# Kernel tuning notes

Measured on AMD Instinct MI355X. Metric: run time of the kernel, lower is better.

## Reference

```python
import jax, jax.numpy as jnp
import numpy as np


def setup_inputs() -> dict:
    key = jax.random.key(0)
    ks = jax.random.split(key, 6)
    B, L, N, C, D = 8, 512, 2048, 1024, 128
    return {
        "teacher_logits": jax.random.normal(ks[0], (B, L, N), dtype=jnp.float32),
        "teacher_features": jax.random.normal(ks[1], (B, N, C), dtype=jnp.float32),
        "Wq": jax.random.normal(ks[2], (D, C), dtype=jnp.float32) * (1.0 / np.sqrt(C)),
        "bq": jnp.zeros((D,), dtype=jnp.float32),
        "Wk": jax.random.normal(ks[3], (D, C), dtype=jnp.float32) * (1.0 / np.sqrt(C)),
        "bk": jnp.zeros((D,), dtype=jnp.float32),
    }


def reference(teacher_logits, teacher_features, Wq, bq, Wk, bk):
    # Linear projections (torch nn.Linear: x @ W^T + b)
    query = jnp.einsum("bnc,dc->bnd", teacher_features, Wq) + bq  # [B,N,D]
    key = jnp.einsum("bnc,dc->bnd", teacher_features, Wk) + bk    # [B,N,D]
    energy = jnp.einsum("bnd,bmd->bnm", query, key)               # [B,N,N]
    attention = jax.nn.softmax(energy, axis=-1)                   # softmax over last dim
    # x_m = teacher_logits @ attention^T : [B,L,N] x [B,N,N]^T -> [B,L,N]
    x_m = jnp.einsum("bln,bmn->blm", teacher_logits, attention)
    return x_m
```

## Files before the change

### kernel.cpp

```cpp
#include <hip/hip_runtime.h>
#include <hip/hip_bf16.h>

#define B_ 8
#define L_ 512
#define N_ 2048
#define C_ 1024
#define D_ 128

typedef __attribute__((ext_vector_type(8))) short    short8;
typedef __attribute__((ext_vector_type(8))) _Float16 half8;
typedef __attribute__((ext_vector_type(4))) float    floatx4;

static __device__ __forceinline__ float s2f(short s) {
    return __uint_as_float(((unsigned)(unsigned short)s) << 16);
}
static __device__ __forceinline__ short f2bf(float f) {
    union { __hip_bfloat16 h; short s; } u;
    u.h = __float2bfloat16(f);
    return u.s;
}

struct F8 { float v[8]; };

static __device__ __forceinline__ F8 load8(const void* raw, long off, int is_bf16) {
    F8 r;
    if (is_bf16) {
        short8 x = *reinterpret_cast<const short8*>((const short*)raw + off);
        #pragma unroll
        for (int i = 0; i < 8; ++i) r.v[i] = s2f(x[i]);
    } else {
        const float* p = (const float*)raw + off;
        float4 a = *reinterpret_cast<const float4*>(p);
        float4 b = *reinterpret_cast<const float4*>(p + 4);
        r.v[0]=a.x; r.v[1]=a.y; r.v[2]=a.z; r.v[3]=a.w;
        r.v[4]=b.x; r.v[5]=b.y; r.v[6]=b.z; r.v[7]=b.w;
    }
    return r;
}

static __device__ __forceinline__ float bias_at(const void* raw, int d, int is_bf16) {
    return is_bf16 ? s2f(((const short*)raw)[d]) : ((const float*)raw)[d];
}

static __device__ __forceinline__ void load_lds16(const void* g, void* l) {
    __builtin_amdgcn_global_load_lds(
        (const __attribute__((address_space(1))) void*)g,
        (__attribute__((address_space(3))) void*)l, 16, 0, 0);
}

__global__ void detect_kernel(const unsigned* __restrict__ words, int* __restrict__ flag) {
    int cnt = 0;
    for (int i = threadIdx.x; i < 256; i += 64) {
        float lowv = __uint_as_float(words[i] << 16);
        float a = fabsf(lowv);
        if (a >= 1e-5f && a <= 100.0f) cnt++;
    }
    #pragma unroll
    for (int off = 32; off; off >>= 1) cnt += __shfl_down(cnt, off);
    if (threadIdx.x == 0) flag[0] = (cnt > 128) ? 1 : 0;
}

__global__ __launch_bounds__(1024) void zero_kernel(float* __restrict__ Z, int n) {
    int i = blockIdx.x * 1024 + threadIdx.x;
    if (i < n) Z[i] = 0.0f;
}

__global__ __launch_bounds__(256) void cvt_kernel(const void* __restrict__ in_raw,
                                                  short* __restrict__ out, long n,
                                                  const int* __restrict__ flag) {
    if (*flag) return;
    long i = ((long)blockIdx.x * 256 + threadIdx.x) * 8;
    if (i >= n) return;
    F8 x = load8(in_raw, i, 0);
    short8 o;
    #pragma unroll
    for (int j = 0; j < 8; ++j) o[j] = f2bf(x.v[j]);
    *reinterpret_cast<short8*>(out + i) = o;
}

__global__ __launch_bounds__(256) void cvt_half_kernel(const void* __restrict__ in_raw,
                                                       _Float16* __restrict__ out, long n,
                                                       const int* __restrict__ flag) {
    if (*flag) return;
    long i = ((long)blockIdx.x * 256 + threadIdx.x) * 8;
    if (i >= n) return;
    F8 x = load8(in_raw, i, 0);
    half8 o;
    #pragma unroll
    for (int j = 0; j < 8; ++j) o[j] = (_Float16)x.v[j];
    *reinterpret_cast<half8*>(out + i) = o;
}

__global__ __launch_bounds__(512) void proj_kernel(
    const void* __restrict__ Fraw,
    const void* __restrict__ Wq_raw, const void* __restrict__ Wk_raw,
    const _Float16* __restrict__ Wq_h, const _Float16* __restrict__ Wk_h,
    const void* __restrict__ bq_raw, const void* __restrict__ bk_raw,
    _Float16* __restrict__ Q, _Float16* __restrict__ K,
    const int* __restrict__ flag)
{
    const int is_bf16 = *flag;
    const int tid  = threadIdx.x;
    const int wave = tid >> 6;
    const int lane = tid & 63;
    const int quad = lane >> 4;
    const int l16  = lane & 15;
    const long r0  = (long)blockIdx.x * 64;

    const int m0   = (wave & 1) * 32;
    const int col0 = (wave >> 1) * 64;

    __shared__ short Ft[64 * 32];
    __shared__ short Wt[256 * 32];

    floatx4 acc[2][4] = {};

    const int srow = lane >> 2;
    const int sg   = (lane & 3) ^ ((srow >> 1) & 3);
    const int skoff = sg * 8;

    if (is_bf16) {
        const short* Fr  = (const short*)Fraw;
        const short* Wqr = (const short*)Wq_raw;
        const short* Wkr = (const short*)Wk_raw;
        for (int kb = 0; kb < 32; ++kb) {
            const int k0 = kb * 32;
            #pragma unroll
            for (int jj = 0; jj < 2; ++jj) {
                const int c = wave * 2 + jj;
                const short* Wr = (c < 8) ? Wqr : Wkr;
                const int wrow = (c & 7) * 16 + srow;
                load_lds16(Wr + (long)wrow * C_ + k0 + skoff,
                           Wt + c * 512 + lane * 8);
            }
            if (wave < 4) {
                load_lds16(Fr + (r0 + wave * 16 + srow) * (long)C_ + k0 + skoff,
                           Ft + wave * 512 + lane * 8);
            }
            __syncthreads();

            short8 af[2], bfr[4];
            #pragma unroll
            for (int t = 0; t < 2; ++t) {
                const int row = m0 + t * 16 + l16;
                const int ph  = quad ^ ((row >> 1) & 3);
                af[t] = *reinterpret_cast<const short8*>(Ft + row * 32 + ph * 8);
            }
            #pragma unroll
            for (int u = 0; u < 4; ++u) {
                const int wrow = col0 + u * 16 + l16;
                const int ph   = quad ^ ((wrow >> 1) & 3);
                bfr[u] = *reinterpret_cast<const short8*>(Wt + wrow * 32 + ph * 8);
            }
            #pragma unroll
            for (int t = 0; t < 2; ++t)
                #pragma unroll
                for (int u = 0; u < 4; ++u)
                    acc[t][u] = __builtin_amdgcn_mfma_f32_16x16x32_bf16(af[t], bfr[u], acc[t][u], 0, 0, 0);
            __syncthreads();
        }
    } else {
        _Float16* Fth = (_Float16*)Ft;
        _Float16* Wth = (_Float16*)Wt;
        for (int kb = 0; kb < 32; ++kb) {
            const int k0 = kb * 32;
            #pragma unroll
            for (int jj = 0; jj < 2; ++jj) {
                const int c = wave * 2 + jj;
                const _Float16* Wh = (c < 8) ? Wq_h : Wk_h;
                const int wrow = (c & 7) * 16 + srow;
                load_lds16(Wh + (long)wrow * C_ + k0 + skoff,
                           Wth + c * 512 + lane * 8);
            }
            if (tid < 256) {
                const int frow = tid >> 2;
                const int fg   = (tid & 3) ^ ((frow >> 1) & 3);
                F8 x = load8(Fraw, (r0 + frow) * (long)C_ + k0 + fg * 8, 0);
                half8 h;
                #pragma unroll
                for (int j = 0; j < 8; ++j) h[j] = (_Float16)x.v[j];
                *reinterpret_cast<half8*>(Fth + tid * 8) = h;
            }
            __syncthreads();

            half8 af[2], bfr[4];
            #pragma unroll
            for (int t = 0; t < 2; ++t) {
                const int row = m0 + t * 16 + l16;
                const int ph  = quad ^ ((row >> 1) & 3);
                af[t] = *reinterpret_cast<const half8*>(Fth + row * 32 + ph * 8);
            }
            #pragma unroll
            for (int u = 0; u < 4; ++u) {
                const int wrow = col0 + u * 16 + l16;
                const int ph   = quad ^ ((wrow >> 1) & 3);
                bfr[u] = *reinterpret_cast<const half8*>(Wth + wrow * 32 + ph * 8);
            }
            #pragma unroll
            for (int t = 0; t < 2; ++t)
                #pragma unroll
                for (int u = 0; u < 4; ++u)
                    acc[t][u] = __builtin_amdgcn_mfma_f32_16x16x32_f16(af[t], bfr[u], acc[t][u], 0, 0, 0);
            __syncthreads();
        }
    }

    const bool isK = (col0 >= 128);
    const void* braw = isK ? bk_raw : bq_raw;
    _Float16* Out    = isK ? K : Q;
    #pragma unroll
    for (int u = 0; u < 4; ++u) {
        const int d = (col0 + u * 16 + l16) & 127;
        const float bv = bias_at(braw, d, is_bf16);
        #pragma unroll
        for (int t = 0; t < 2; ++t)
            #pragma unroll
            for (int r = 0; r < 4; ++r) {
                const long row = r0 + m0 + t * 16 + quad * 4 + r;
                Out[row * D_ + d] = (_Float16)(acc[t][u][r] + bv);
            }
    }
}

__global__ __launch_bounds__(512) void attn_pz_kernel(
    const _Float16* __restrict__ Q,
    const _Float16* __restrict__ K,
    short* __restrict__ P,
    float* __restrict__ Z)
{
    const int b    = blockIdx.y;
    const int i0   = blockIdx.x * 32;
    const int wave = threadIdx.x >> 6;
    const int lane = threadIdx.x & 63;
    const int quad = lane >> 4;
    const int l16  = lane & 15;

    const _Float16* Qb = Q + (long)b * N_ * D_;
    const _Float16* Kb = K + (long)b * N_ * D_;

    half8 a[2][4];
    #pragma unroll
    for (int v = 0; v < 2; ++v)
        #pragma unroll
        for (int s = 0; s < 4; ++s)
            a[v][s] = *reinterpret_cast<const half8*>(
                Qb + (long)(i0 + v * 16 + l16) * D_ + s * 32 + quad * 8);

    const int jbase = wave * 256;
    short* Pb = P + (long)b * N_ * N_;

    float zpart[2][4] = {};

    #pragma unroll
    for (int t = 0; t < 16; ++t) {
        const _Float16* krow = Kb + (long)(jbase + t * 16 + l16) * D_ + quad * 8;
        floatx4 acc[2] = {};
        #pragma unroll
        for (int s = 0; s < 4; ++s) {
            half8 kf = *reinterpret_cast<const half8*>(krow + s * 32);
            acc[0] = __builtin_amdgcn_mfma_f32_16x16x32_f16(a[0][s], kf, acc[0], 0, 0, 0);
            acc[1] = __builtin_amdgcn_mfma_f32_16x16x32_f16(a[1][s], kf, acc[1], 0, 0, 0);
        }
        const int j = jbase + t * 16 + l16;
        #pragma unroll
        for (int v = 0; v < 2; ++v)
            #pragma unroll
            for (int r = 0; r < 4; ++r) {
                float e = __expf(acc[v][r]);
                zpart[v][r] += e;
                Pb[(long)(i0 + v * 16 + quad * 4 + r) * N_ + j] = f2bf(e);
            }
    }

    #pragma unroll
    for (int v = 0; v < 2; ++v)
        #pragma unroll
        for (int r = 0; r < 4; ++r) {
            float z = zpart[v][r];
            z += __shfl_xor(z, 1);
            z += __shfl_xor(z, 2);
            z += __shfl_xor(z, 4);
            z += __shfl_xor(z, 8);
            if (l16 == 0)
                atomicAdd(&Z[(long)b * N_ + i0 + v * 16 + quad * 4 + r], z);
        }
}

__global__ __launch_bounds__(256) void xm_kernel(
    const void* __restrict__ Lraw,
    const short* __restrict__ Lcvt,
    const short* __restrict__ A,
    const float* __restrict__ Z,
    void* __restrict__ OutRaw,
    const int* __restrict__ flag)
{
    const int is_bf16 = *flag;
    const int b  = blockIdx.z;
    const int r0 = blockIdx.x * 128;
    const int c0 = blockIdx.y * 128;
    const int wave = threadIdx.x >> 6;
    const int lane = threadIdx.x & 63;
    const int quad = lane >> 4;
    const int l16  = lane & 15;

    __shared__ short Atile[128 * 64];
    __shared__ short Btile[128 * 64];

    const short* Lb = (is_bf16 ? (const short*)Lraw : Lcvt) + (long)b * L_ * N_;
    const short* Ab = A + (long)b * N_ * N_;

    const int m0 = (wave & 1) * 64;
    const int n0 = (wave >> 1) * 64;

    floatx4 acc[4][4] = {};

    const int srow  = lane >> 3;
    const int skoff = ((lane & 7) ^ srow) * 8;

    for (int kb = 0; kb < 32; ++kb) {
        const int k0 = kb * 64;
        #pragma unroll
        for (int j = 0; j < 8; ++j) {
            const int cc = wave * 8 + j;
            if (cc < 16) {
                const short* src = Lb + (long)(r0 + cc * 8 + srow) * N_ + k0 + skoff;
                load_lds16(src, Atile + cc * 512);
            } else {
                const int c8 = cc - 16;
                const short* src = Ab + (long)(c0 + c8 * 8 + srow) * N_ + k0 + skoff;
                load_lds16(src, Btile + c8 * 512);
            }
        }
        __syncthreads();

        #pragma unroll
        for (int ks = 0; ks < 2; ++ks) {
            short8 af[4], bf[4];
            #pragma unroll
            for (int t = 0; t < 4; ++t) {
                const int row = m0 + t * 16 + l16;
                const int ph  = (ks * 4 + quad) ^ (row & 7);
                af[t] = *reinterpret_cast<const short8*>(Atile + row * 64 + ph * 8);
            }
            #pragma unroll
            for (int u = 0; u < 4; ++u) {
                const int row = n0 + u * 16 + l16;
                const int ph  = (ks * 4 + quad) ^ (row & 7);
                bf[u] = *reinterpret_cast<const short8*>(Btile + row * 64 + ph * 8);
            }
            #pragma unroll
            for (int t = 0; t < 4; ++t)
                #pragma unroll
                for (int u = 0; u < 4; ++u)
                    acc[t][u] = __builtin_amdgcn_mfma_f32_16x16x32_bf16(af[t], bf[u], acc[t][u], 0, 0, 0);
        }
        __syncthreads();
    }

    float invz[4];
    #pragma unroll
    for (int u = 0; u < 4; ++u)
        invz[u] = 1.0f / Z[(long)b * N_ + c0 + n0 + u * 16 + l16];

    if (is_bf16) {
        short* Ob = (short*)OutRaw + (long)b * L_ * N_;
        #pragma unroll
        for (int t = 0; t < 4; ++t)
            #pragma unroll
            for (int u = 0; u < 4; ++u)
                #pragma unroll
                for (int r = 0; r < 4; ++r) {
                    const long row = r0 + m0 + t * 16 + quad * 4 + r;
                    const int  col = c0 + n0 + u * 16 + l16;
                    Ob[row * N_ + col] = f2bf(acc[t][u][r] * invz[u]);
                }
    } else {
        float* Ob = (float*)OutRaw + (long)b * L_ * N_;
        #pragma unroll
        for (int t = 0; t < 4; ++t)
            #pragma unroll
            for (int u = 0; u < 4; ++u)
                #pragma unroll
                for (int r = 0; r < 4; ++r) {
                    const long row = r0 + m0 + t * 16 + quad * 4 + r;
                    const int  col = c0 + n0 + u * 16 + l16;
                    Ob[row * N_ + col] = acc[t][u][r] * invz[u];
                }
    }
}

extern "C" void kernel_launch(void* const* d_in, const int* in_sizes, int n_in,
                              void* d_out, int out_size, void* d_ws, size_t ws_size,
                              hipStream_t stream) {
    const void* logits_raw = d_in[0];
    const void* feats_raw  = d_in[1];
    const void* wq_raw     = d_in[2];
    const void* bq_raw     = d_in[3];
    const void* wk_raw     = d_in[4];
    const void* bk_raw     = d_in[5];

    char* ws = (char*)d_ws;
    size_t off = 0;
    int* flag = (int*)(ws + off);           off += 256;
    short* logb = (short*)(ws + off);       off += (size_t)B_ * L_ * N_ * 2;
    _Float16* Wq_h = (_Float16*)(ws + off); off += (size_t)D_ * C_ * 2;
    _Float16* Wk_h = (_Float16*)(ws + off); off += (size_t)D_ * C_ * 2;
    _Float16* Q = (_Float16*)(ws + off);    off += (size_t)B_ * N_ * D_ * 2;
    _Float16* K = (_Float16*)(ws + off);    off += (size_t)B_ * N_ * D_ * 2;
    float* Z = (float*)(ws + off);          off += (size_t)B_ * N_ * 4;
    short* A = (short*)(ws + off);          off += (size_t)B_ * N_ * N_ * 2;

    hipLaunchKernelGGL(detect_kernel, dim3(1), dim3(64), 0, stream,
                       (const unsigned*)feats_raw, flag);
    hipLaunchKernelGGL(zero_kernel, dim3((B_ * N_ + 1023) / 1024), dim3(1024), 0, stream,
                       Z, B_ * N_);
    hipLaunchKernelGGL(cvt_kernel, dim3((B_ * L_ * N_) / (256 * 8)), dim3(256), 0, stream,
                       logits_raw, logb, (long)B_ * L_ * N_, flag);
    hipLaunchKernelGGL(cvt_half_kernel, dim3((D_ * C_) / (256 * 8)), dim3(256), 0, stream,
                       wq_raw, Wq_h, (long)D_ * C_, flag);
    hipLaunchKernelGGL(cvt_half_kernel, dim3((D_ * C_) / (256 * 8)), dim3(256), 0, stream,
                       wk_raw, Wk_h, (long)D_ * C_, flag);
    hipLaunchKernelGGL(proj_kernel, dim3(B_ * N_ / 64), dim3(512), 0, stream,
                       feats_raw, wq_raw, wk_raw, Wq_h, Wk_h, bq_raw, bk_raw, Q, K, flag);
    hipLaunchKernelGGL(attn_pz_kernel, dim3(N_ / 32, B_), dim3(512), 0, stream,
                       Q, K, A, Z);
    hipLaunchKernelGGL(xm_kernel, dim3(L_ / 128, N_ / 128, B_), dim3(256), 0, stream,
                       logits_raw, logb, A, Z, d_out, flag);
}
```

Baseline: 265.0 us.

## Fuse attention exp and logits matmul into one kernel with LDS P tiles

Replaces the separate attention kernel, which wrote a full B×N×N bf16 exp matrix to global memory, and the xm GEMM that read it back, with a single flash-style kernel. Each block computes exp(QK^T) for a 64-column slice in 128-wide chunks, stores them in double-buffered LDS, and immediately multiplies them with logits rows loaded directly from global memory into registers. The row sums Z are accumulated in shared memory, which also removes the zero kernel and the global atomics. The cost is that the logits are re-read per column block without LDS staging, the block count is small (256), and there is only one barrier per chunk with double buffering, so correctness depends on the two-buffer spacing.

```diff
diff --git a/kernel.cpp b/kernel.cpp
--- a/kernel.cpp
+++ b/kernel.cpp
@@ -8,6 +8,7 @@
 #define D_ 128
 
 typedef __attribute__((ext_vector_type(8))) short    short8;
+typedef __attribute__((ext_vector_type(4))) short    short4v;
 typedef __attribute__((ext_vector_type(8))) _Float16 half8;
 typedef __attribute__((ext_vector_type(4))) float    floatx4;
 
@@ -58,11 +59,6 @@
     #pragma unroll
     for (int off = 32; off; off >>= 1) cnt += __shfl_down(cnt, off);
     if (threadIdx.x == 0) flag[0] = (cnt > 128) ? 1 : 0;
-}
-
-__global__ __launch_bounds__(1024) void zero_kernel(float* __restrict__ Z, int n) {
-    int i = blockIdx.x * 1024 + threadIdx.x;
-    if (i < n) Z[i] = 0.0f;
 }
 
 __global__ __launch_bounds__(256) void cvt_kernel(const void* __restrict__ in_raw,
@@ -222,145 +218,115 @@
     }
 }
 
-__global__ __launch_bounds__(512) void attn_pz_kernel(
+__global__ __launch_bounds__(512, 2) void fused_attn_xm_kernel(
+    const void* __restrict__ Lraw,
+    const short* __restrict__ Lcvt,
     const _Float16* __restrict__ Q,
     const _Float16* __restrict__ K,
-    short* __restrict__ P,
-    float* __restrict__ Z)
+    void* __restrict__ OutRaw,
+    const int* __restrict__ flag)
 {
-    const int b    = blockIdx.y;
-    const int i0   = blockIdx.x * 32;
+    const int is_bf16 = *flag;
+    const int f    = blockIdx.y * 32 + blockIdx.x;
+    const int b    = f & 7;
+    const int m0   = (f >> 3) * 64;
     const int wave = threadIdx.x >> 6;
     const int lane = threadIdx.x & 63;
     const int quad = lane >> 4;
     const int l16  = lane & 15;
 
+    __shared__ short P0[64 * 128];
+    __shared__ short P1[64 * 128];
+    __shared__ float Zs[64];
+
+    if (threadIdx.x < 64) Zs[threadIdx.x] = 0.0f;
+
+    const short*    Lb = (is_bf16 ? (const short*)Lraw : Lcvt) + (long)b * L_ * N_;
     const _Float16* Qb = Q + (long)b * N_ * D_;
     const _Float16* Kb = K + (long)b * N_ * D_;
 
-    half8 a[2][4];
-    #pragma unroll
-    for (int v = 0; v < 2; ++v)
+    half8 bq[4][4];
+    #pragma unroll
+    for (int u = 0; u < 4; ++u)
         #pragma unroll
         for (int s = 0; s < 4; ++s)
-            a[v][s] = *reinterpret_cast<const half8*>(
-                Qb + (long)(i0 + v * 16 + l16) * D_ + s * 32 + quad * 8);
-
-    const int jbase = wave * 256;
-    short* Pb = P + (long)b * N_ * N_;
-
-    float zpart[2][4] = {};
-
-    #pragma unroll
-    for (int t = 0; t < 16; ++t) {
-        const _Float16* krow = Kb + (long)(jbase + t * 16 + l16) * D_ + quad * 8;
-        floatx4 acc[2] = {};
+            bq[u][s] = *reinterpret_cast<const half8*>(
+                Qb + (long)(m0 + u * 16 + l16) * D_ + s * 32 + quad * 8);
+
+    const int lw  = wave * 64;
+    const int swz = l16 * 2;
+
+    floatx4 acc[4][4] = {};
+    float zpart[4] = {};
+
+    #pragma unroll 2
+    for (int ch = 0; ch < 16; ++ch) {
+        const int n0 = ch * 128;
+        short* Pb = (ch & 1) ? P1 : P0;
+
+        const _Float16* krow = Kb + (long)(n0 + wave * 16 + l16) * D_ + quad * 8;
+        floatx4 ae[4] = {};
         #pragma unroll
         for (int s = 0; s < 4; ++s) {
             half8 kf = *reinterpret_cast<const half8*>(krow + s * 32);
-            acc[0] = __builtin_amdgcn_mfma_f32_16x16x32_f16(a[0][s], kf, acc[0], 0, 0, 0);
-            acc[1] = __builtin_amdgcn_mfma_f32_16x16x32_f16(a[1][s], kf, acc[1], 0, 0, 0);
-        }
-        const int j = jbase + t * 16 + l16;
-        #pragma unroll
-        for (int v = 0; v < 2; ++v)
+            #pragma unroll
+            for (int u = 0; u < 4; ++u)
+                ae[u] = __builtin_amdgcn_mfma_f32_16x16x32_f16(kf, bq[u][s], ae[u], 0, 0, 0);
+        }
+
+        short8 al[4][4];
+        #pragma unroll
+        for (int t = 0; t < 4; ++t)
+            #pragma unroll
+            for (int ks = 0; ks < 4; ++ks)
+                al[t][ks] = *reinterpret_cast<const short8*>(
+                    Lb + (long)(lw + t * 16 + l16) * N_ + n0 + ks * 32 + quad * 8);
+
+        #pragma unroll
+        for (int u = 0; u < 4; ++u) {
+            short4v pk;
             #pragma unroll
             for (int r = 0; r < 4; ++r) {
-                float e = __expf(acc[v][r]);
-                zpart[v][r] += e;
-                Pb[(long)(i0 + v * 16 + quad * 4 + r) * N_ + j] = f2bf(e);
-            }
-    }
-
-    #pragma unroll
-    for (int v = 0; v < 2; ++v)
-        #pragma unroll
-        for (int r = 0; r < 4; ++r) {
-            float z = zpart[v][r];
-            z += __shfl_xor(z, 1);
-            z += __shfl_xor(z, 2);
-            z += __shfl_xor(z, 4);
-            z += __shfl_xor(z, 8);
-            if (l16 == 0)
-                atomicAdd(&Z[(long)b * N_ + i0 + v * 16 + quad * 4 + r], z);
-        }
-}
-
-__global__ __launch_bounds__(256) void xm_kernel(
-    const void* __restrict__ Lraw,
-    const short* __restrict__ Lcvt,
-    const short* __restrict__ A,
-    const float* __restrict__ Z,
-    void* __restrict__ OutRaw,
-    const int* __restrict__ flag)
-{
-    const int is_bf16 = *flag;
-    const int b  = blockIdx.z;
-    const int r0 = blockIdx.x * 128;
-    const int c0 = blockIdx.y * 128;
-    const int wave = threadIdx.x >> 6;
-    const int lane = threadIdx.x & 63;
-    const int quad = lane >> 4;
-    const int l16  = lane & 15;
-
-    __shared__ short Atile[128 * 64];
-    __shared__ short Btile[128 * 64];
-
-    const short* Lb = (is_bf16 ? (const short*)Lraw : Lcvt) + (long)b * L_ * N_;
-    const short* Ab = A + (long)b * N_ * N_;
-
-    const int m0 = (wave & 1) * 64;
-    const int n0 = (wave >> 1) * 64;
-
-    floatx4 acc[4][4] = {};
-
-    const int srow  = lane >> 3;
-    const int skoff = ((lane & 7) ^ srow) * 8;
-
-    for (int kb = 0; kb < 32; ++kb) {
-        const int k0 = kb * 64;
-        #pragma unroll
-        for (int j = 0; j < 8; ++j) {
-            const int cc = wave * 8 + j;
-            if (cc < 16) {
-                const short* src = Lb + (long)(r0 + cc * 8 + srow) * N_ + k0 + skoff;
-                load_lds16(src, Atile + cc * 512);
-            } else {
-                const int c8 = cc - 16;
-                const short* src = Ab + (long)(c0 + c8 * 8 + srow) * N_ + k0 + skoff;
-                load_lds16(src, Btile + c8 * 512);
-            }
+                float e = __expf(ae[u][r]);
+                zpart[u] += e;
+                pk[r] = f2bf(e);
+            }
+            const int m = u * 16 + l16;
+            *reinterpret_cast<short4v*>(
+                Pb + m * 128 + (((wave * 4 + quad) ^ swz) << 2)) = pk;
         }
         __syncthreads();
 
         #pragma unroll
-        for (int ks = 0; ks < 2; ++ks) {
-            short8 af[4], bf[4];
-            #pragma unroll
-            for (int t = 0; t < 4; ++t) {
-                const int row = m0 + t * 16 + l16;
-                const int ph  = (ks * 4 + quad) ^ (row & 7);
-                af[t] = *reinterpret_cast<const short8*>(Atile + row * 64 + ph * 8);
-            }
+        for (int ks = 0; ks < 4; ++ks) {
+            short8 bp[4];
             #pragma unroll
             for (int u = 0; u < 4; ++u) {
-                const int row = n0 + u * 16 + l16;
-                const int ph  = (ks * 4 + quad) ^ (row & 7);
-                bf[u] = *reinterpret_cast<const short8*>(Btile + row * 64 + ph * 8);
+                const int m = u * 16 + l16;
+                bp[u] = *reinterpret_cast<const short8*>(
+                    Pb + m * 128 + ((((ks * 8 + quad * 2) ^ swz)) << 2));
             }
             #pragma unroll
             for (int t = 0; t < 4; ++t)
                 #pragma unroll
                 for (int u = 0; u < 4; ++u)
-                    acc[t][u] = __builtin_amdgcn_mfma_f32_16x16x32_bf16(af[t], bf[u], acc[t][u], 0, 0, 0);
-        }
-        __syncthreads();
-    }
+                    acc[t][u] = __builtin_amdgcn_mfma_f32_16x16x32_bf16(
+                        al[t][ks], bp[u], acc[t][u], 0, 0, 0);
+        }
+    }
+
+    #pragma unroll
+    for (int u = 0; u < 4; ++u) {
+        float z = zpart[u];
+        z += __shfl_xor(z, 16);
+        z += __shfl_xor(z, 32);
+        if (lane < 16) atomicAdd(&Zs[u * 16 + lane], z);
+    }
+    __syncthreads();
 
     float invz[4];
     #pragma unroll
-    for (int u = 0; u < 4; ++u)
-        invz[u] = 1.0f / Z[(long)b * N_ + c0 + n0 + u * 16 + l16];
+    for (int u = 0; u < 4; ++u) invz[u] = 1.0f / Zs[u * 16 + l16];
 
     if (is_bf16) {
         short* Ob = (short*)OutRaw + (long)b * L_ * N_;
@@ -370,8 +336,8 @@
             for (int u = 0; u < 4; ++u)
                 #pragma unroll
                 for (int r = 0; r < 4; ++r) {
-                    const long row = r0 + m0 + t * 16 + quad * 4 + r;
-                    const int  col = c0 + n0 + u * 16 + l16;
+                    const long row = lw + t * 16 + quad * 4 + r;
+                    const int  col = m0 + u * 16 + l16;
                     Ob[row * N_ + col] = f2bf(acc[t][u][r] * invz[u]);
                 }
     } else {
@@ -382,8 +348,8 @@
             for (int u = 0; u < 4; ++u)
                 #pragma unroll
                 for (int r = 0; r < 4; ++r) {
-                    const long row = r0 + m0 + t * 16 + quad * 4 + r;
-                    const int  col = c0 + n0 + u * 16 + l16;
+                    const long row = lw + t * 16 + quad * 4 + r;
+                    const int  col = m0 + u * 16 + l16;
                     Ob[row * N_ + col] = acc[t][u][r] * invz[u];
                 }
     }
@@ -407,13 +373,9 @@
     _Float16* Wk_h = (_Float16*)(ws + off); off += (size_t)D_ * C_ * 2;
     _Float16* Q = (_Float16*)(ws + off);    off += (size_t)B_ * N_ * D_ * 2;
     _Float16* K = (_Float16*)(ws + off);    off += (size_t)B_ * N_ * D_ * 2;
-    float* Z = (float*)(ws + off);          off += (size_t)B_ * N_ * 4;
-    short* A = (short*)(ws + off);          off += (size_t)B_ * N_ * N_ * 2;
 
     hipLaunchKernelGGL(detect_kernel, dim3(1), dim3(64), 0, stream,
                        (const unsigned*)feats_raw, flag);
-    hipLaunchKernelGGL(zero_kernel, dim3((B_ * N_ + 1023) / 1024), dim3(1024), 0, stream,
-                       Z, B_ * N_);
     hipLaunchKernelGGL(cvt_kernel, dim3((B_ * L_ * N_) / (256 * 8)), dim3(256), 0, stream,
                        logits_raw, logb, (long)B_ * L_ * N_, flag);
     hipLaunchKernelGGL(cvt_half_kernel, dim3((D_ * C_) / (256 * 8)), dim3(256), 0, stream,
@@ -422,8 +384,6 @@
                        wk_raw, Wk_h, (long)D_ * C_, flag);
     hipLaunchKernelGGL(proj_kernel, dim3(B_ * N_ / 64), dim3(512), 0, stream,
                        feats_raw, wq_raw, wk_raw, Wq_h, Wk_h, bq_raw, bk_raw, Q, K, flag);
-    hipLaunchKernelGGL(attn_pz_kernel, dim3(N_ / 32, B_), dim3(512), 0, stream,
-                       Q, K, A, Z);
-    hipLaunchKernelGGL(xm_kernel, dim3(L_ / 128, N_ / 128, B_), dim3(256), 0, stream,
-                       logits_raw, logb, A, Z, d_out, flag);
-}
+    hipLaunchKernelGGL(fused_attn_xm_kernel, dim3(N_ / 64, B_), dim3(512), 0, stream,
+                       logits_raw, logb, Q, K, d_out, flag);
+}
```

Result: faster. 246.1 us (-7.1%).
